# Performance work log

Measured on AMD Instinct MI355X. Metric: run time of the kernel, lower is better.

Reference implementation:

```python
import jax, jax.numpy as jnp
import numpy as np

B, N, D = 256, 196, 1024   # batch, regions, vis_embed_dim
HID, ATT, SIN, WID, ISD = 1024, 256, 1024, 1024, 256
S = 10                      # sentence steps


def _lin(key, out_dim, in_dim):
    kw, kb = jax.random.split(key)
    w = jax.random.normal(kw, (out_dim, in_dim), jnp.float32) * 0.02
    b = jax.random.normal(kb, (out_dim,), jnp.float32) * 0.02
    return w, b


def setup_inputs() -> dict:
    key = jax.random.key(0)
    ks = jax.random.split(key, 16)
    inp = {}
    inp['vis_enc'] = jax.random.normal(ks[0], (B, N, D), jnp.float32)
    inp['sentences'] = jax.random.randint(ks[1], (B, S, 50), 0, 10000, jnp.int64)
    inp['enc_att_w'], inp['enc_att_b'] = _lin(ks[2], ATT, D)
    inp['dec_att_w'], inp['dec_att_b'] = _lin(ks[3], ATT, HID)
    inp['full_att_w'], inp['full_att_b'] = _lin(ks[4], 1, ATT)
    inp['ctx_w'], inp['ctx_b'] = _lin(ks[5], SIN, D)
    inp['W_ih'], inp['b_ih'] = _lin(ks[6], 4 * HID, SIN)
    inp['W_hh'], inp['b_hh'] = _lin(ks[7], 4 * HID, HID)
    inp['topic_hid_w'], inp['topic_hid_b'] = _lin(ks[8], WID, HID)
    inp['topic_ctx_w'], inp['topic_ctx_b'] = _lin(ks[9], WID, SIN)
    inp['stop_prev_w'], inp['stop_prev_b'] = _lin(ks[10], ISD, HID)
    inp['stop_cur_w'], inp['stop_cur_b'] = _lin(ks[11], ISD, HID)
    inp['final_stop_w'], inp['final_stop_b'] = _lin(ks[12], 2, ISD)
    return inp


def reference(vis_enc, sentences,
              enc_att_w, enc_att_b, dec_att_w, dec_att_b, full_att_w, full_att_b,
              ctx_w, ctx_b, W_ih, b_ih, W_hh, b_hh,
              topic_hid_w, topic_hid_b, topic_ctx_w, topic_ctx_b,
              stop_prev_w, stop_prev_b, stop_cur_w, stop_cur_b,
              final_stop_w, final_stop_b):
    batch, hid = vis_enc.shape[0], W_hh.shape[1]
    sent_num = sentences.shape[1]
    # encoder projection is h-independent -> hoist out of the recurrence
    vis_enc_att = jnp.einsum('bnd,ad->bna', vis_enc, enc_att_w) + enc_att_b  # [B,N,ATT]

    def step(carry, _):
        h, c = carry
        # CoAtt additive attention
        dec = h @ dec_att_w.T + dec_att_b                       # [B,ATT]
        join = jnp.tanh(vis_enc_att + dec[:, None, :])          # [B,N,ATT]
        logits = jnp.einsum('bna,a->bn', join, full_att_w[0]) + full_att_b[0]
        scores = jax.nn.softmax(logits, axis=1)                 # [B,N]
        att_out = jnp.einsum('bn,bnd->bd', scores, vis_enc)     # [B,D]
        ctx = att_out @ ctx_w.T + ctx_b                         # [B,SIN]
        h_prev = h
        # LSTMCell
        gates = ctx @ W_ih.T + b_ih + h @ W_hh.T + b_hh         # [B,4H]
        i, f, g, o = jnp.split(gates, 4, axis=1)
        c_new = jax.nn.sigmoid(f) * c + jax.nn.sigmoid(i) * jnp.tanh(g)
        h_new = jax.nn.sigmoid(o) * jnp.tanh(c_new)
        # topic + stop heads
        topic = jnp.tanh(h_new @ topic_hid_w.T + topic_hid_b
                         + ctx @ topic_ctx_w.T + topic_ctx_b)   # [B,WID]
        p = jnp.tanh(h_prev @ stop_prev_w.T + stop_prev_b
                     + h_new @ stop_cur_w.T + stop_cur_b)
        p = p @ final_stop_w.T + final_stop_b                   # [B,2]
        return (h_new, c_new), (topic, p)

    h0 = jnp.zeros((batch, hid), vis_enc.dtype)
    c0 = jnp.zeros((batch, hid), vis_enc.dtype)
    _, (topics, ps) = jax.lax.scan(step, (h0, c0), None, length=sent_num)
    topics = jnp.transpose(topics, (1, 0, 2))  # [B,S,WID]
    ps = jnp.transpose(ps, (1, 0, 2))          # [B,S,2]
    return topics, ps
```

## Files before the change

### kernel.cpp

```cpp
#include <hip/hip_runtime.h>
#include <hip/hip_bf16.h>
#include <math.h>

static constexpr int BB = 256;
static constexpr int NR = 196;
static constexpr int DV = 1024;
static constexpr int HH = 1024;
static constexpr int AT = 256;
static constexpr int SI = 1024;
static constexpr int WI = 1024;
static constexpr int IS = 256;
static constexpr int ST = 10;

__device__ __forceinline__ float sigmoidf_(float x) { return 1.0f / (1.0f + expf(-x)); }

__device__ __forceinline__ ushort f2bf(float x) {
    uint u = __float_as_uint(x);
    return (ushort)((u + 0x7FFFu + ((u >> 16) & 1u)) >> 16);
}
__device__ __forceinline__ float bf2f(ushort b) { return __uint_as_float(((uint)b) << 16); }

using bf16x8 = __attribute__((ext_vector_type(8))) short;
using f32x4  = __attribute__((ext_vector_type(4))) float;
#define MFMA_B16(a, b, c) __builtin_amdgcn_mfma_f32_16x16x32_bf16((a), (b), (c), 0, 0, 0)

__device__ __forceinline__ void split8(const float4& u, const float4& v, uint4& hq, uint4& lq) {
    ushort h0 = f2bf(u.x), h1 = f2bf(u.y), h2 = f2bf(u.z), h3 = f2bf(u.w);
    ushort h4 = f2bf(v.x), h5 = f2bf(v.y), h6 = f2bf(v.z), h7 = f2bf(v.w);
    hq.x = h0 | ((uint)h1 << 16); hq.y = h2 | ((uint)h3 << 16);
    hq.z = h4 | ((uint)h5 << 16); hq.w = h6 | ((uint)h7 << 16);
    ushort l0 = f2bf(u.x - bf2f(h0)), l1 = f2bf(u.y - bf2f(h1));
    ushort l2 = f2bf(u.z - bf2f(h2)), l3 = f2bf(u.w - bf2f(h3));
    ushort l4 = f2bf(v.x - bf2f(h4)), l5 = f2bf(v.y - bf2f(h5));
    ushort l6 = f2bf(v.z - bf2f(h6)), l7 = f2bf(v.w - bf2f(h7));
    lq.x = l0 | ((uint)l1 << 16); lq.y = l2 | ((uint)l3 << 16);
    lq.z = l4 | ((uint)l5 << 16); lq.w = l6 | ((uint)l7 << 16);
}

struct CvtTab { const float* s[5]; ushort* h[5]; ushort* l[5]; };

__global__ __launch_bounds__(256) void convert_split(CvtTab tab) {
    const int cum[6] = {0, 256, 4352, 5376, 5632, 5888};
    const int bid = blockIdx.x;
    int seg = 0;
#pragma unroll
    for (int i = 1; i < 5; ++i) if (bid >= cum[i]) seg = i;
    const float* s = tab.s[seg];
    ushort* h = tab.h[seg];
    ushort* l = tab.l[seg];
    const int r = bid - cum[seg];
    int rd = r;
    if (seg == 1) rd = (r & 1023) * 4 + (r >> 10);
    const int src = r * 1024 + threadIdx.x * 4;
    const size_t dst = (size_t)rd * 1024 + threadIdx.x * 4;
    float4 v = *(const float4*)(s + src);
    ushort h0 = f2bf(v.x), h1 = f2bf(v.y), h2 = f2bf(v.z), h3 = f2bf(v.w);
    uint2 hq, lq;
    hq.x = h0 | ((uint)h1 << 16); hq.y = h2 | ((uint)h3 << 16);
    ushort l0 = f2bf(v.x - bf2f(h0)), l1 = f2bf(v.y - bf2f(h1));
    ushort l2 = f2bf(v.z - bf2f(h2)), l3 = f2bf(v.w - bf2f(h3));
    lq.x = l0 | ((uint)l1 << 16); lq.y = l2 | ((uint)l3 << 16);
    *(uint2*)(h + dst) = hq;
    *(uint2*)(l + dst) = lq;
}

__global__ __launch_bounds__(256) void convert_vis(
    const float* __restrict__ src, ushort* __restrict__ dst)
{
    const size_t i = ((size_t)blockIdx.x * 256 + threadIdx.x) * 8;
    const float4 v0 = *(const float4*)(src + i);
    const float4 v1 = *(const float4*)(src + i + 4);
    uint4 o;
    o.x = f2bf(v0.x) | ((uint)f2bf(v0.y) << 16);
    o.y = f2bf(v0.z) | ((uint)f2bf(v0.w) << 16);
    o.z = f2bf(v1.x) | ((uint)f2bf(v1.y) << 16);
    o.w = f2bf(v1.z) | ((uint)f2bf(v1.w) << 16);
    *(uint4*)(dst + i) = o;
}

__global__ __launch_bounds__(256) void transpose_split(
    const float* __restrict__ src, ushort* __restrict__ dh, ushort* __restrict__ dl)
{
    __shared__ float T[32][33];
    const int tx = threadIdx.x & 31, ty = threadIdx.x >> 5;
    const int k0 = blockIdx.x * 32, n0 = blockIdx.y * 32;
#pragma unroll
    for (int j = 0; j < 4; ++j)
        T[ty + 8 * j][tx] = src[(size_t)(k0 + ty + 8 * j) * 1024 + n0 + tx];
    __syncthreads();
#pragma unroll
    for (int j = 0; j < 4; ++j) {
        const float v = T[tx][ty + 8 * j];
        const ushort h = f2bf(v);
        const size_t o = (size_t)(n0 + ty + 8 * j) * 1024 + k0 + tx;
        dh[o] = h;
        dl[o] = f2bf(v - bf2f(h));
    }
}

__global__ __launch_bounds__(256) void foldbias(
    const float* __restrict__ W, const float* __restrict__ v,
    const float* __restrict__ b, float* __restrict__ out)
{
    const int n = blockIdx.x * 4 + (threadIdx.x >> 6);
    const int lane = threadIdx.x & 63;
    const float* wr = W + (size_t)n * 1024;
    float p = 0.f;
#pragma unroll
    for (int i = 0; i < 4; ++i) {
        const float4 wv = *(const float4*)&wr[i * 256 + lane * 4];
        const float4 vv = *(const float4*)&v[i * 256 + lane * 4];
        p = fmaf(wv.x, vv.x, p); p = fmaf(wv.y, vv.y, p);
        p = fmaf(wv.z, vv.z, p); p = fmaf(wv.w, vv.w, p);
    }
    for (int off = 32; off; off >>= 1) p += __shfl_down(p, off);
    if (lane == 0) out[n] = p + b[n];
}

template <int ILV>
__global__ __launch_bounds__(256) void mgemm_ws(
    const float* __restrict__ A, const ushort* __restrict__ Wh, const ushort* __restrict__ Wl,
    ushort* __restrict__ Ch, ushort* __restrict__ Cl, int N, int K)
{
    __shared__ __align__(16) ushort SM[4 * 64 * 40];
    ushort* Ah = SM; ushort* Al = SM + 2560; ushort* Bh = SM + 5120; ushort* Bl = SM + 7680;

    const int t = threadIdx.x;
    const int m0 = blockIdx.y * 64, n0 = blockIdx.x * 64;
    const int w = t >> 6, lane = t & 63;
    const int l15 = lane & 15, q = lane >> 4;
    const int sr = t >> 2, sq = (t & 3) * 8;
    const int nch = K >> 5;

    f32x4 acc[4] = {};
    float4 pa0, pa1; uint4 pbh, pbl;
    auto pref = [&](int c) {
        const int k0 = c << 5;
        const float* ap = &A[(size_t)(m0 + sr) * K + k0 + sq];
        pa0 = *(const float4*)ap;
        pa1 = *(const float4*)(ap + 4);
        pbh = *(const uint4*)&Wh[(size_t)(n0 + sr) * K + k0 + sq];
        pbl = *(const uint4*)&Wl[(size_t)(n0 + sr) * K + k0 + sq];
    };
    pref(0);

    for (int c = 0; c < nch; ++c) {
        __syncthreads();
        uint4 hq, lq; split8(pa0, pa1, hq, lq);
        *(uint4*)&Ah[sr * 40 + sq] = hq;
        *(uint4*)&Al[sr * 40 + sq] = lq;
        *(uint4*)&Bh[sr * 40 + sq] = pbh;
        *(uint4*)&Bl[sr * 40 + sq] = pbl;
        __syncthreads();
        if (c + 1 < nch) pref(c + 1);
        const bf16x8 bh = *(const bf16x8*)&Bh[(w * 16 + l15) * 40 + q * 8];
        const bf16x8 bl = *(const bf16x8*)&Bl[(w * 16 + l15) * 40 + q * 8];
#pragma unroll
        for (int mi = 0; mi < 4; ++mi) {
            const bf16x8 ah = *(const bf16x8*)&Ah[(mi * 16 + l15) * 40 + q * 8];
            const bf16x8 al = *(const bf16x8*)&Al[(mi * 16 + l15) * 40 + q * 8];
            acc[mi] = MFMA_B16(ah, bh, acc[mi]);
            acc[mi] = MFMA_B16(ah, bl, acc[mi]);
            acc[mi] = MFMA_B16(al, bh, acc[mi]);
        }
    }

    const int col = n0 + w * 16 + l15;
#pragma unroll
    for (int mi = 0; mi < 4; ++mi) {
#pragma unroll
        for (int j = 0; j < 4; ++j) {
            const int row = m0 + mi * 16 + q * 4 + j;
            const int ro = ILV ? ((row & 1023) * 4 + (row >> 10)) : row;
            const float v = acc[mi][j];
            const ushort h = f2bf(v);
            Ch[(size_t)ro * N + col] = h;
            Cl[(size_t)ro * N + col] = f2bf(v - bf2f(h));
        }
    }
}

template <int EPI, int DUAL, int OMAP>
__global__ __launch_bounds__(256) void mgemm(
    const float* __restrict__ A1, const ushort* __restrict__ W1h, const ushort* __restrict__ W1l,
    const float* __restrict__ b1,
    const float* __restrict__ A2, const ushort* __restrict__ W2h, const ushort* __restrict__ W2l,
    const float* __restrict__ b2,
    float* __restrict__ C, int M, int N, int K, int ldc)
{
    __shared__ __align__(16) ushort SM[4 * 64 * 40];
    ushort* Ah = SM; ushort* Al = SM + 2560; ushort* Bh = SM + 5120; ushort* Bl = SM + 7680;

    const int t = threadIdx.x;
    const int m0 = blockIdx.y * 64, n0 = blockIdx.x * 64;
    const int w = t >> 6, lane = t & 63;
    const int l15 = lane & 15, q = lane >> 4;
    const int sr = t >> 2, sq = (t & 3) * 8;
    const int KC = K >> 5, nch = (DUAL ? 2 : 1) * KC;

    f32x4 acc[4] = {};
    float4 pa0, pa1; uint4 pbh, pbl;

    auto pref = [&](int c) {
        const int pass = DUAL ? (c >= KC ? 1 : 0) : 0;
        const int k0 = (c - pass * KC) << 5;
        const float* A = pass ? A2 : A1;
        const ushort* Wh = pass ? W2h : W1h;
        const ushort* Wl = pass ? W2l : W1l;
        const float* ap = &A[(size_t)(m0 + sr) * K + k0 + sq];
        pa0 = *(const float4*)ap;
        pa1 = *(const float4*)(ap + 4);
        pbh = *(const uint4*)&Wh[(size_t)(n0 + sr) * K + k0 + sq];
        pbl = *(const uint4*)&Wl[(size_t)(n0 + sr) * K + k0 + sq];
    };
    pref(0);

    for (int c = 0; c < nch; ++c) {
        __syncthreads();
        uint4 hq, lq; split8(pa0, pa1, hq, lq);
        *(uint4*)&Ah[sr * 40 + sq] = hq;
        *(uint4*)&Al[sr * 40 + sq] = lq;
        *(uint4*)&Bh[sr * 40 + sq] = pbh;
        *(uint4*)&Bl[sr * 40 + sq] = pbl;
        __syncthreads();
        if (c + 1 < nch) pref(c + 1);
        const bf16x8 bh = *(const bf16x8*)&Bh[(w * 16 + l15) * 40 + q * 8];
        const bf16x8 bl = *(const bf16x8*)&Bl[(w * 16 + l15) * 40 + q * 8];
#pragma unroll
        for (int mi = 0; mi < 4; ++mi) {
            const bf16x8 ah = *(const bf16x8*)&Ah[(mi * 16 + l15) * 40 + q * 8];
            const bf16x8 al = *(const bf16x8*)&Al[(mi * 16 + l15) * 40 + q * 8];
            acc[mi] = MFMA_B16(ah, bh, acc[mi]);
            acc[mi] = MFMA_B16(ah, bl, acc[mi]);
            acc[mi] = MFMA_B16(al, bh, acc[mi]);
        }
    }

    const int col = n0 + w * 16 + l15;
    float bias = b1[col];
    if (DUAL) bias += b2[col];
#pragma unroll
    for (int mi = 0; mi < 4; ++mi) {
#pragma unroll
        for (int j = 0; j < 4; ++j) {
            const int row = m0 + mi * 16 + q * 4 + j;
            float v = acc[mi][j] + bias;
            if (EPI == 1) v = tanhf(v);
            if (OMAP)
                C[((size_t)(row & 255) * ST + (row >> 8)) * ldc + col] = v;
            else
                C[(size_t)row * ldc + col] = v;
        }
    }
}

__global__ __launch_bounds__(512) void mgemm8_lstm(
    const ushort* __restrict__ A1h, const ushort* __restrict__ A1l,
    const ushort* __restrict__ W1h, const ushort* __restrict__ W1l,
    const float* __restrict__ b1,
    const ushort* __restrict__ A2h, const ushort* __restrict__ A2l,
    const ushort* __restrict__ W2h, const ushort* __restrict__ W2l,
    const float* __restrict__ b2,
    int K, float* __restrict__ cvec, float* __restrict__ hnew,
    ushort* __restrict__ hnh, ushort* __restrict__ hnl)
{
    __shared__ __align__(16) ushort SM[32256];

    const int t = threadIdx.x;
    const int m0 = blockIdx.y * 64, n0 = blockIdx.x * 32;
    const int w = t >> 6, lane = t & 63;
    const int g = w >> 2, wg = w & 3;
    const int l15 = lane & 15, q = lane >> 4;
    const int tl = t & 255;
    const int sr = tl >> 2, sq4 = (tl & 3) * 16;
    const int br = tl >> 3, bq = (tl & 7) * 8;
    const int mh = wg >> 1;
    const int colL = (wg & 1) * 16 + l15;

    ushort* Ah = SM + g * 13824;
    ushort* Al = Ah + 4608;
    ushort* Bh = Al + 4608;
    ushort* Bl = Bh + 2304;

    const int nchg = K >> 6;
    const ushort* Ahg = g ? A2h : A1h;
    const ushort* Alg = g ? A2l : A1l;
    const ushort* Wh  = g ? W2h : W1h;
    const ushort* Wl  = g ? W2l : W1l;

    f32x4 acc[2] = {};
    uint4 pah0, pah1, pal0, pal1, pbh, pbl;
    auto pref = [&](int c) {
        const int k0 = c << 6;
        const size_t ab = (size_t)(m0 + sr) * K + k0 + sq4;
        pah0 = *(const uint4*)&Ahg[ab];
        pah1 = *(const uint4*)&Ahg[ab + 8];
        pal0 = *(const uint4*)&Alg[ab];
        pal1 = *(const uint4*)&Alg[ab + 8];
        pbh = *(const uint4*)&Wh[(size_t)(n0 + br) * K + k0 + bq];
        pbl = *(const uint4*)&Wl[(size_t)(n0 + br) * K + k0 + bq];
    };
    pref(0);

    for (int c = 0; c < nchg; ++c) {
        __syncthreads();
        *(uint4*)&Ah[sr * 72 + sq4]     = pah0;
        *(uint4*)&Ah[sr * 72 + sq4 + 8] = pah1;
        *(uint4*)&Al[sr * 72 + sq4]     = pal0;
        *(uint4*)&Al[sr * 72 + sq4 + 8] = pal1;
        *(uint4*)&Bh[br * 72 + bq] = pbh;
        *(uint4*)&Bl[br * 72 + bq] = pbl;
        __syncthreads();
        if (c + 1 < nchg) pref(c + 1);
#pragma unroll
        for (int ks = 0; ks < 2; ++ks) {
            const bf16x8 bh = *(const bf16x8*)&Bh[colL * 72 + ks * 32 + q * 8];
            const bf16x8 bl = *(const bf16x8*)&Bl[colL * 72 + ks * 32 + q * 8];
#pragma unroll
            for (int i = 0; i < 2; ++i) {
                const int mi = mh * 2 + i;
                const bf16x8 ah = *(const bf16x8*)&Ah[(mi * 16 + l15) * 72 + ks * 32 + q * 8];
                const bf16x8 al = *(const bf16x8*)&Al[(mi * 16 + l15) * 72 + ks * 32 + q * 8];
                acc[i] = MFMA_B16(ah, bh, acc[i]);
                acc[i] = MFMA_B16(ah, bl, acc[i]);
                acc[i] = MFMA_B16(al, bh, acc[i]);
            }
        }
    }

    float* comb = (float*)(SM + 27648);
    __syncthreads();
    if (g == 1) {
#pragma unroll
        for (int i = 0; i < 2; ++i)
#pragma unroll
            for (int j = 0; j < 4; ++j) comb[tl * 9 + i * 4 + j] = acc[i][j];
    }
    __syncthreads();
    if (g == 0) {
#pragma unroll
        for (int i = 0; i < 2; ++i)
#pragma unroll
            for (int j = 0; j < 4; ++j) acc[i][j] += comb[tl * 9 + i * 4 + j];
    }

    float* G = (float*)(SM + 13824);
    if (g == 0) {
        const int colG = n0 + colL;
        const int gate = colG & 3, unit = colG >> 2;
        const float bias = b1[gate * 1024 + unit] + b2[gate * 1024 + unit];
#pragma unroll
        for (int i = 0; i < 2; ++i) {
            const int mi = mh * 2 + i;
#pragma unroll
            for (int j = 0; j < 4; ++j)
                G[(mi * 16 + q * 4 + j) * 40 + colL] = acc[i][j] + bias;
        }
    }
    __syncthreads();
    {
        const int row = t >> 3, ul = t & 7;
        const float4 g4 = *(const float4*)&G[row * 40 + ul * 4];
        const size_t ci = (size_t)(m0 + row) * HH + (n0 >> 2) + ul;
        const float cn = sigmoidf_(g4.y) * cvec[ci] + sigmoidf_(g4.x) * tanhf(g4.z);
        cvec[ci] = cn;
        const float hv = sigmoidf_(g4.w) * tanhf(cn);
        hnew[ci] = hv;
        const ushort hhi = f2bf(hv);
        hnh[ci] = hhi;
        hnl[ci] = f2bf(hv - bf2f(hhi));
    }
}

__global__ __launch_bounds__(512) void mgemm_preb(
    const ushort* __restrict__ vh, const ushort* __restrict__ Wh, const ushort* __restrict__ Wl,
    const float* __restrict__ bias, ushort* __restrict__ C)
{
    __shared__ __align__(16) ushort Avh[128 * 40];
    __shared__ __align__(16) ushort Bh[256 * 40];
    __shared__ __align__(16) ushort Bl[256 * 40];

    const int t = threadIdx.x;
    const int m0 = blockIdx.x * 128;
    const int w = t >> 6, lane = t & 63;
    const int rg = w >> 2, cg = w & 3;
    const int l15 = lane & 15, q = lane >> 4;
    const int ar = t >> 2, ac = (t & 3) * 8;
    const int brr = t >> 1, bc = (t & 1) * 16;
    const int K = DV;

    f32x4 acc[4][4] = {};
    uint4 pa, pbh0, pbh1, pbl0, pbl1;
    auto pref = [&](int c) {
        const int k0 = c << 5;
        pa   = *(const uint4*)&vh[(size_t)(m0 + ar) * K + k0 + ac];
        const size_t bb = (size_t)brr * K + k0 + bc;
        pbh0 = *(const uint4*)&Wh[bb];
        pbh1 = *(const uint4*)&Wh[bb + 8];
        pbl0 = *(const uint4*)&Wl[bb];
        pbl1 = *(const uint4*)&Wl[bb + 8];
    };
    pref(0);

    for (int c = 0; c < 32; ++c) {
        __syncthreads();
        *(uint4*)&Avh[ar * 40 + ac] = pa;
        *(uint4*)&Bh[brr * 40 + bc]     = pbh0;
        *(uint4*)&Bh[brr * 40 + bc + 8] = pbh1;
        *(uint4*)&Bl[brr * 40 + bc]     = pbl0;
        *(uint4*)&Bl[brr * 40 + bc + 8] = pbl1;
        __syncthreads();
        if (c + 1 < 32) pref(c + 1);

        bf16x8 ah[4];
#pragma unroll
        for (int mi = 0; mi < 4; ++mi)
            ah[mi] = *(const bf16x8*)&Avh[(rg * 64 + mi * 16 + l15) * 40 + q * 8];
#pragma unroll
        for (int ni = 0; ni < 4; ++ni) {
            const bf16x8 bh = *(const bf16x8*)&Bh[(cg * 64 + ni * 16 + l15) * 40 + q * 8];
            const bf16x8 bl = *(const bf16x8*)&Bl[(cg * 64 + ni * 16 + l15) * 40 + q * 8];
#pragma unroll
            for (int mi = 0; mi < 4; ++mi) {
                acc[mi][ni] = MFMA_B16(ah[mi], bh, acc[mi][ni]);
                acc[mi][ni] = MFMA_B16(ah[mi], bl, acc[mi][ni]);
            }
        }
    }

#pragma unroll
    for (int ni = 0; ni < 4; ++ni) {
        const int col = cg * 64 + ni * 16 + l15;
        const float bb = bias[col];
#pragma unroll
        for (int mi = 0; mi < 4; ++mi)
#pragma unroll
            for (int j = 0; j < 4; ++j) {
                const int row = m0 + rg * 64 + mi * 16 + q * 4 + j;
                C[(size_t)row * AT + col] = f2bf(acc[mi][ni][j] + bb);
            }
    }
}

__global__ __launch_bounds__(256) void mgemm_pre(
    const float* __restrict__ A, const ushort* __restrict__ Wh, const ushort* __restrict__ Wl,
    const float* __restrict__ bias, ushort* __restrict__ C)
{
    __shared__ __align__(16) ushort Ah[64 * 40], Al[64 * 40];
    __shared__ __align__(16) ushort Bh[256 * 40], Bl[256 * 40];

    const int t = threadIdx.x;
    const int m0 = blockIdx.x * 64;
    const int w = t >> 6, lane = t & 63;
    const int l15 = lane & 15, q = lane >> 4;
    const int sr = t >> 2, sq = (t & 3) * 8;
    const int K = DV;

    f32x4 acc[4][4] = {};
    float4 pa0, pa1;
    auto prefA = [&](int k0) {
        const float* ap = &A[(size_t)(m0 + sr) * K + k0 + sq];
        pa0 = *(const float4*)ap;
        pa1 = *(const float4*)(ap + 4);
    };
    prefA(0);

    for (int c = 0; c < 32; ++c) {
        const int k0 = c << 5;
        __syncthreads();
        uint4 hq, lq; split8(pa0, pa1, hq, lq);
        *(uint4*)&Ah[sr * 40 + sq] = hq;
        *(uint4*)&Al[sr * 40 + sq] = lq;
#pragma unroll
        for (int i = 0; i < 4; ++i) {
            const int r = sr + 64 * i;
            *(uint4*)&Bh[r * 40 + sq] = *(const uint4*)&Wh[(size_t)r * K + k0 + sq];
            *(uint4*)&Bl[r * 40 + sq] = *(const uint4*)&Wl[(size_t)r * K + k0 + sq];
        }
        __syncthreads();
        if (c + 1 < 32) prefA((c + 1) << 5);

        bf16x8 ah[4], al[4];
#pragma unroll
        for (int mi = 0; mi < 4; ++mi) {
            ah[mi] = *(const bf16x8*)&Ah[(mi * 16 + l15) * 40 + q * 8];
            al[mi] = *(const bf16x8*)&Al[(mi * 16 + l15) * 40 + q * 8];
        }
#pragma unroll
        for (int ni = 0; ni < 4; ++ni) {
            const bf16x8 bh = *(const bf16x8*)&Bh[(w * 64 + ni * 16 + l15) * 40 + q * 8];
            const bf16x8 bl = *(const bf16x8*)&Bl[(w * 64 + ni * 16 + l15) * 40 + q * 8];
#pragma unroll
            for (int mi = 0; mi < 4; ++mi) {
                acc[mi][ni] = MFMA_B16(ah[mi], bh, acc[mi][ni]);
                acc[mi][ni] = MFMA_B16(ah[mi], bl, acc[mi][ni]);
                acc[mi][ni] = MFMA_B16(al[mi], bh, acc[mi][ni]);
            }
        }
    }

#pragma unroll
    for (int ni = 0; ni < 4; ++ni) {
        const int col = w * 64 + ni * 16 + l15;
        const float bb = bias[col];
#pragma unroll
        for (int mi = 0; mi < 4; ++mi)
#pragma unroll
            for (int j = 0; j < 4; ++j) {
                const int row = m0 + mi * 16 + q * 4 + j;
                C[(size_t)row * AT + col] = f2bf(acc[mi][ni][j] + bb);
            }
    }
}

template <int VBF>
__global__ __launch_bounds__(1024) void att_step(
    const ushort* __restrict__ vis_att, const float* __restrict__ h,
    const float* __restrict__ dec_w, const float* __restrict__ dec_b,
    const float* __restrict__ fw, const float* __restrict__ fbp,
    const void* __restrict__ visp, float* __restrict__ att_out,
    ushort* __restrict__ att_h, ushort* __restrict__ att_l)
{
    const int b = blockIdx.x;
    const int t = threadIdx.x;
    const int lane = t & 63;
    const int w = t >> 6;

    __shared__ float hs[HH];
    __shared__ float decs[AT];
    __shared__ float fwv[AT];
    __shared__ float logit[NR + 4];
    __shared__ float sc[NR + 4];
    __shared__ float red[8];
    __shared__ float part[8][DV];

    hs[t] = h[(size_t)b * HH + t];
    if (t < AT) fwv[t] = fw[t];
    __syncthreads();
    const float fb = fbp[0];

#pragma unroll
    for (int j = 0; j < 16; ++j) {
        const int a = w * 16 + j;
        const float* wr = dec_w + (size_t)a * HH;
        float p = 0.f;
#pragma unroll
        for (int i = 0; i < 4; ++i) {
            const float4 wv = *(const float4*)&wr[i * 256 + lane * 4];
            const float4 hv = *(const float4*)&hs[i * 256 + lane * 4];
            p = fmaf(wv.x, hv.x, p); p = fmaf(wv.y, hv.y, p);
            p = fmaf(wv.z, hv.z, p); p = fmaf(wv.w, hv.w, p);
        }
        for (int off = 32; off; off >>= 1) p += __shfl_down(p, off);
        if (lane == 0) decs[a] = p + dec_b[a];
    }
    __syncthreads();

    for (int n = w; n < NR; n += 16) {
        const ushort4 v4 = *(const ushort4*)&vis_att[((size_t)b * NR + n) * AT + lane * 4];
        const int a = lane * 4;
        float s = tanhf(bf2f(v4.x) + decs[a]) * fwv[a];
        s = fmaf(tanhf(bf2f(v4.y) + decs[a + 1]), fwv[a + 1], s);
        s = fmaf(tanhf(bf2f(v4.z) + decs[a + 2]), fwv[a + 2], s);
        s = fmaf(tanhf(bf2f(v4.w) + decs[a + 3]), fwv[a + 3], s);
        for (int off = 32; off; off >>= 1) s += __shfl_down(s, off);
        if (lane == 0) logit[n] = s + fb;
    }
    __syncthreads();

    float m = -1e30f, e = 0.f;
    if (t < NR) m = logit[t];
    if (t < 256) {
        for (int off = 32; off; off >>= 1) m = fmaxf(m, __shfl_down(m, off));
        if (lane == 0) red[w] = m;
    }
    __syncthreads();
    m = fmaxf(fmaxf(red[0], red[1]), fmaxf(red[2], red[3]));
    if (t < NR) e = expf(logit[t] - m);
    if (t < 256) {
        float ss = e;
        for (int off = 32; off; off >>= 1) ss += __shfl_down(ss, off);
        if (lane == 0) red[4 + w] = ss;
    }
    __syncthreads();
    const float S = red[4] + red[5] + red[6] + red[7];
    if (t < NR) sc[t] = e / S;
    __syncthreads();

    const int slice = t >> 7;
    const int c8 = (t & 127) * 8;
    const int nbeg = (slice <= 4) ? 25 * slice : 100 + 24 * (slice - 4);
    const int nend = (slice < 4) ? nbeg + 25 : nbeg + 24;
    float a0 = 0.f, a1 = 0.f, a2 = 0.f, a3 = 0.f;
    float a4 = 0.f, a5 = 0.f, a6 = 0.f, a7 = 0.f;
    if (VBF) {
        const ushort* vb = (const ushort*)visp + (size_t)b * NR * DV + c8;
        for (int n = nbeg; n < nend; ++n) {
            const float s = sc[n];
            const uint4 v = *(const uint4*)&vb[(size_t)n * DV];
            a0 = fmaf(s, bf2f((ushort)(v.x & 0xFFFF)), a0);
            a1 = fmaf(s, bf2f((ushort)(v.x >> 16)), a1);
            a2 = fmaf(s, bf2f((ushort)(v.y & 0xFFFF)), a2);
            a3 = fmaf(s, bf2f((ushort)(v.y >> 16)), a3);
            a4 = fmaf(s, bf2f((ushort)(v.z & 0xFFFF)), a4);
            a5 = fmaf(s, bf2f((ushort)(v.z >> 16)), a5);
            a6 = fmaf(s, bf2f((ushort)(v.w & 0xFFFF)), a6);
            a7 = fmaf(s, bf2f((ushort)(v.w >> 16)), a7);
        }
    } else {
        const float* vb = (const float*)visp + (size_t)b * NR * DV + c8;
        for (int n = nbeg; n < nend; ++n) {
            const float s = sc[n];
            const float4 v0 = *(const float4*)&vb[(size_t)n * DV];
            const float4 v1 = *(const float4*)&vb[(size_t)n * DV + 4];
            a0 = fmaf(s, v0.x, a0); a1 = fmaf(s, v0.y, a1);
            a2 = fmaf(s, v0.z, a2); a3 = fmaf(s, v0.w, a3);
            a4 = fmaf(s, v1.x, a4); a5 = fmaf(s, v1.y, a5);
            a6 = fmaf(s, v1.z, a6); a7 = fmaf(s, v1.w, a7);
        }
    }
    float4 av0; av0.x = a0; av0.y = a1; av0.z = a2; av0.w = a3;
    float4 av1; av1.x = a4; av1.y = a5; av1.z = a6; av1.w = a7;
    *(float4*)&part[slice][c8]     = av0;
    *(float4*)&part[slice][c8 + 4] = av1;
    __syncthreads();
    const float v = ((part[0][t] + part[1][t]) + (part[2][t] + part[3][t]))
                  + ((part[4][t] + part[5][t]) + (part[6][t] + part[7][t]));
    att_out[(size_t)b * DV + t] = v;
    const ushort vh16 = f2bf(v);
    att_h[(size_t)b * DV + t] = vh16;
    att_l[(size_t)b * DV + t] = f2bf(v - bf2f(vh16));
}

__global__ __launch_bounds__(256) void stop_final_all(
    const float* __restrict__ pt, const float* __restrict__ fw,
    const float* __restrict__ fb, float* __restrict__ outp)
{
    const int row = blockIdx.x;
    const int s = row >> 8, b = row & 255;
    const int t = threadIdx.x;
    const int lane = t & 63;
    const int w = t >> 6;

    __shared__ float red[16];
    const float v = pt[(size_t)row * IS + t];
    float p0 = v * fw[t];
    float p1 = v * fw[IS + t];
    for (int off = 32; off; off >>= 1) {
        p0 += __shfl_down(p0, off);
        p1 += __shfl_down(p1, off);
    }
    if (lane == 0) { red[w] = p0; red[8 + w] = p1; }
    __syncthreads();
    if (t == 0) {
        outp[((size_t)b * ST + s) * 2 + 0] = red[0] + red[1] + red[2] + red[3] + fb[0];
        outp[((size_t)b * ST + s) * 2 + 1] = red[8] + red[9] + red[10] + red[11] + fb[1];
    }
}

extern "C" void kernel_launch(void* const* d_in, const int* in_sizes, int n_in,
                              void* d_out, int out_size, void* d_ws, size_t ws_size,
                              hipStream_t stream)
{
    const float* vis        = (const float*)d_in[0];
    const float* enc_att_w  = (const float*)d_in[2];
    const float* enc_att_b  = (const float*)d_in[3];
    const float* dec_att_w  = (const float*)d_in[4];
    const float* dec_att_b  = (const float*)d_in[5];
    const float* full_att_w = (const float*)d_in[6];
    const float* full_att_b = (const float*)d_in[7];
    const float* ctx_w      = (const float*)d_in[8];
    const float* ctx_b      = (const float*)d_in[9];
    const float* W_ih       = (const float*)d_in[10];
    const float* b_ih       = (const float*)d_in[11];
    const float* W_hh       = (const float*)d_in[12];
    const float* b_hh       = (const float*)d_in[13];
    const float* topic_hid_w = (const float*)d_in[14];
    const float* topic_hid_b = (const float*)d_in[15];
    const float* topic_ctx_w = (const float*)d_in[16];
    const float* topic_ctx_b = (const float*)d_in[17];
    const float* stop_prev_w = (const float*)d_in[18];
    const float* stop_prev_b = (const float*)d_in[19];
    const float* stop_cur_w  = (const float*)d_in[20];
    const float* stop_cur_b  = (const float*)d_in[21];
    const float* final_stop_w = (const float*)d_in[22];
    const float* final_stop_b = (const float*)d_in[23];

    float* out_topics = (float*)d_out;
    float* out_ps     = (float*)d_out + (size_t)BB * ST * WI;

    char* ws = (char*)d_ws;
    size_t off = 0;
    auto alloc = [&](size_t bytes) -> void* {
        void* p = (void*)(ws + off);
        off += (bytes + 255) & ~(size_t)255;
        return p;
    };
    ushort* vis_att = (ushort*)alloc((size_t)BB * NR * AT * 2);
    const size_t WTOT = (size_t)5888 * 1024;
    ushort* wh = (ushort*)alloc(WTOT * 2);
    ushort* wl = (ushort*)alloc(WTOT * 2);
    float* h_all   = (float*)alloc((size_t)(ST + 1) * BB * HH * 4);
    ushort* hh_h   = (ushort*)alloc((size_t)(ST + 1) * BB * HH * 2);
    ushort* hh_l   = (ushort*)alloc((size_t)(ST + 1) * BB * HH * 2);
    float* att_all = (float*)alloc((size_t)ST * BB * DV * 4);
    ushort* att_h  = (ushort*)alloc((size_t)BB * DV * 2);
    ushort* att_l  = (ushort*)alloc((size_t)BB * DV * 2);
    float* cbuf    = (float*)alloc((size_t)BB * HH * 4);
    float* pt_all  = (float*)alloc((size_t)ST * BB * IS * 4);
    ushort* ctT_h  = (ushort*)alloc((size_t)SI * DV * 2);
    ushort* ctT_l  = (ushort*)alloc((size_t)SI * DV * 2);
    ushort* cmb_h  = (ushort*)alloc((size_t)4 * HH * SI * 2);
    ushort* cmb_l  = (ushort*)alloc((size_t)4 * HH * SI * 2);
    ushort* tcc_h  = (ushort*)alloc((size_t)WI * SI * 2);
    ushort* tcc_l  = (ushort*)alloc((size_t)WI * SI * 2);
    float* bf_ih   = (float*)alloc((size_t)4 * HH * 4);
    float* bf_tc   = (float*)alloc((size_t)WI * 4);
    if (off > ws_size) return;
    ushort* vis_bf = nullptr;
    {
        const size_t need = (size_t)BB * NR * DV * 2;
        if (off + need <= ws_size) vis_bf = (ushort*)alloc(need);
    }

    const size_t O_ENC = 0;
    const size_t O_HH  = 262144;
    const size_t O_TH  = 4456448;
    const size_t O_SP  = 5505024;
    const size_t O_SC  = 5767168;

    CvtTab tab;
    const float* srcs[5] = {enc_att_w, W_hh, topic_hid_w, stop_prev_w, stop_cur_w};
    const size_t offs[5] = {O_ENC, O_HH, O_TH, O_SP, O_SC};
    for (int i = 0; i < 5; ++i) {
        tab.s[i] = srcs[i];
        tab.h[i] = wh + offs[i];
        tab.l[i] = wl + offs[i];
    }

    hipMemsetAsync(h_all, 0, (size_t)BB * HH * 4, stream);
    hipMemsetAsync(hh_h, 0, (size_t)BB * HH * 2, stream);
    hipMemsetAsync(hh_l, 0, (size_t)BB * HH * 2, stream);
    hipMemsetAsync(cbuf, 0, (size_t)BB * HH * 4, stream);

    convert_split<<<5888, 256, 0, stream>>>(tab);

    transpose_split<<<dim3(SI / 32, DV / 32), 256, 0, stream>>>(ctx_w, ctT_h, ctT_l);
    mgemm_ws<1><<<dim3(SI / 64, 4 * HH / 64), 256, 0, stream>>>(
        W_ih, ctT_h, ctT_l, cmb_h, cmb_l, SI, DV);
    mgemm_ws<0><<<dim3(SI / 64, WI / 64), 256, 0, stream>>>(
        topic_ctx_w, ctT_h, ctT_l, tcc_h, tcc_l, SI, DV);
    foldbias<<<(4 * HH) / 4, 256, 0, stream>>>(W_ih, ctx_b, b_ih, bf_ih);
    foldbias<<<WI / 4, 256, 0, stream>>>(topic_ctx_w, ctx_b, topic_ctx_b, bf_tc);

    if (vis_bf) {
        convert_vis<<<(BB * NR * DV) / (256 * 8), 256, 0, stream>>>(vis, vis_bf);
        mgemm_preb<<<(BB * NR) / 128, 512, 0, stream>>>(
            vis_bf, wh + O_ENC, wl + O_ENC, enc_att_b, vis_att);
    } else {
        mgemm_pre<<<(BB * NR) / 64, 256, 0, stream>>>(
            vis, wh + O_ENC, wl + O_ENC, enc_att_b, vis_att);
    }

    for (int s = 0; s < ST; ++s) {
        float* hc = h_all + (size_t)s * BB * HH;
        float* hn = h_all + (size_t)(s + 1) * BB * HH;
        ushort* hch = hh_h + (size_t)s * BB * HH;
        ushort* hcl = hh_l + (size_t)s * BB * HH;
        ushort* hnh = hh_h + (size_t)(s + 1) * BB * HH;
        ushort* hnl = hh_l + (size_t)(s + 1) * BB * HH;
        float* atts = att_all + (size_t)s * BB * DV;
        if (vis_bf)
            att_step<1><<<BB, 1024, 0, stream>>>(vis_att, hc, dec_att_w, dec_att_b,
                                                 full_att_w, full_att_b, vis_bf, atts,
                                                 att_h, att_l);
        else
            att_step<0><<<BB, 1024, 0, stream>>>(vis_att, hc, dec_att_w, dec_att_b,
                                                 full_att_w, full_att_b, vis, atts,
                                                 att_h, att_l);
        mgemm8_lstm<<<dim3(4 * HH / 32, BB / 64), 512, 0, stream>>>(
            att_h, att_l, cmb_h, cmb_l, bf_ih,
            hch, hcl, wh + O_HH, wl + O_HH, b_hh,
            SI, cbuf, hn, hnh, hnl);
    }

    mgemm<1, 1, 1><<<dim3(WI / 64, (ST * BB) / 64), 256, 0, stream>>>(
        h_all + (size_t)BB * HH, wh + O_TH, wl + O_TH, topic_hid_b,
        att_all, tcc_h, tcc_l, bf_tc,
        out_topics, ST * BB, WI, HH, WI);
    mgemm<1, 1, 0><<<dim3(IS / 64, (ST * BB) / 64), 256, 0, stream>>>(
        h_all, wh + O_SP, wl + O_SP, stop_prev_b,
        h_all + (size_t)BB * HH, wh + O_SC, wl + O_SC, stop_cur_b,
        pt_all, ST * BB, IS, HH, IS);
    stop_final_all<<<ST * BB, 256, 0, stream>>>(pt_all, final_stop_w, final_stop_b, out_ps);
}
```

Measured before the change: 1.073 ms.

## Reuse pre-split bf16 activations in head GEMMs and swizzle LSTM weight LDS

The topic and stop head GEMMs now read the pre-split bf16 hi/lo copies of h and the attention output instead of fp32 inputs, so the per-chunk split conversion disappears. Attention output is stored only as bf16 hi/lo per step, which drops the fp32 att_all write. The LSTM GEMM B tile gets an XOR-swizzled LDS layout with no padding, a smaller shared footprint and a launch_bounds occupancy hint. The fp32 fallback path is removed, so the bf16 vis workspace must now always be available.

New measurement: 1.035 ms. -3.6%, faster.

```diff
diff --git a/kernel.cpp b/kernel.cpp
--- a/kernel.cpp
+++ b/kernel.cpp
@@ -180,13 +180,15 @@
     }
 }
 
-template <int EPI, int DUAL, int OMAP>
-__global__ __launch_bounds__(256) void mgemm(
-    const float* __restrict__ A1, const ushort* __restrict__ W1h, const ushort* __restrict__ W1l,
+template <int OMAP>
+__global__ __launch_bounds__(256) void mgemm_ps(
+    const ushort* __restrict__ A1h, const ushort* __restrict__ A1l,
+    const ushort* __restrict__ W1h, const ushort* __restrict__ W1l,
     const float* __restrict__ b1,
-    const float* __restrict__ A2, const ushort* __restrict__ W2h, const ushort* __restrict__ W2l,
+    const ushort* __restrict__ A2h, const ushort* __restrict__ A2l,
+    const ushort* __restrict__ W2h, const ushort* __restrict__ W2l,
     const float* __restrict__ b2,
-    float* __restrict__ C, int M, int N, int K, int ldc)
+    float* __restrict__ C, int N, int K, int ldc)
 {
     __shared__ __align__(16) ushort SM[4 * 64 * 40];
     ushort* Ah = SM; ushort* Al = SM + 2560; ushort* Bh = SM + 5120; ushort* Bl = SM + 7680;
@@ -196,20 +198,21 @@
     const int w = t >> 6, lane = t & 63;
     const int l15 = lane & 15, q = lane >> 4;
     const int sr = t >> 2, sq = (t & 3) * 8;
-    const int KC = K >> 5, nch = (DUAL ? 2 : 1) * KC;
+    const int KC = K >> 5, nch = 2 * KC;
 
     f32x4 acc[4] = {};
-    float4 pa0, pa1; uint4 pbh, pbl;
+    uint4 pah, pal, pbh, pbl;
 
     auto pref = [&](int c) {
-        const int pass = DUAL ? (c >= KC ? 1 : 0) : 0;
+        const int pass = (c >= KC) ? 1 : 0;
         const int k0 = (c - pass * KC) << 5;
-        const float* A = pass ? A2 : A1;
+        const ushort* Axh = pass ? A2h : A1h;
+        const ushort* Axl = pass ? A2l : A1l;
         const ushort* Wh = pass ? W2h : W1h;
         const ushort* Wl = pass ? W2l : W1l;
-        const float* ap = &A[(size_t)(m0 + sr) * K + k0 + sq];
-        pa0 = *(const float4*)ap;
-        pa1 = *(const float4*)(ap + 4);
+        const size_t ab = (size_t)(m0 + sr) * K + k0 + sq;
+        pah = *(const uint4*)&Axh[ab];
+        pal = *(const uint4*)&Axl[ab];
         pbh = *(const uint4*)&Wh[(size_t)(n0 + sr) * K + k0 + sq];
         pbl = *(const uint4*)&Wl[(size_t)(n0 + sr) * K + k0 + sq];
     };
@@ -217,9 +220,8 @@
 
     for (int c = 0; c < nch; ++c) {
         __syncthreads();
-        uint4 hq, lq; split8(pa0, pa1, hq, lq);
-        *(uint4*)&Ah[sr * 40 + sq] = hq;
-        *(uint4*)&Al[sr * 40 + sq] = lq;
+        *(uint4*)&Ah[sr * 40 + sq] = pah;
+        *(uint4*)&Al[sr * 40 + sq] = pal;
         *(uint4*)&Bh[sr * 40 + sq] = pbh;
         *(uint4*)&Bl[sr * 40 + sq] = pbl;
         __syncthreads();
@@ -237,15 +239,13 @@
     }
 
     const int col = n0 + w * 16 + l15;
-    float bias = b1[col];
-    if (DUAL) bias += b2[col];
+    const float bias = b1[col] + b2[col];
 #pragma unroll
     for (int mi = 0; mi < 4; ++mi) {
 #pragma unroll
         for (int j = 0; j < 4; ++j) {
             const int row = m0 + mi * 16 + q * 4 + j;
-            float v = acc[mi][j] + bias;
-            if (EPI == 1) v = tanhf(v);
+            const float v = tanhf(acc[mi][j] + bias);
             if (OMAP)
                 C[((size_t)(row & 255) * ST + (row >> 8)) * ldc + col] = v;
             else
@@ -254,7 +254,7 @@
     }
 }
 
-__global__ __launch_bounds__(512) void mgemm8_lstm(
+__global__ __launch_bounds__(512, 6) void mgemm8_lstm(
     const ushort* __restrict__ A1h, const ushort* __restrict__ A1l,
     const ushort* __restrict__ W1h, const ushort* __restrict__ W1l,
     const float* __restrict__ b1,
@@ -264,7 +264,7 @@
     int K, float* __restrict__ cvec, float* __restrict__ hnew,
     ushort* __restrict__ hnh, ushort* __restrict__ hnl)
 {
-    __shared__ __align__(16) ushort SM[32256];
+    __shared__ __align__(16) ushort SM[26624];
 
     const int t = threadIdx.x;
     const int m0 = blockIdx.y * 64, n0 = blockIdx.x * 32;
@@ -277,16 +277,18 @@
     const int mh = wg >> 1;
     const int colL = (wg & 1) * 16 + l15;
 
-    ushort* Ah = SM + g * 13824;
+    ushort* Ah = SM + g * 13312;
     ushort* Al = Ah + 4608;
     ushort* Bh = Al + 4608;
-    ushort* Bl = Bh + 2304;
+    ushort* Bl = Bh + 2048;
 
     const int nchg = K >> 6;
     const ushort* Ahg = g ? A2h : A1h;
     const ushort* Alg = g ? A2l : A1l;
     const ushort* Wh  = g ? W2h : W1h;
     const ushort* Wl  = g ? W2l : W1l;
+
+    const int bwi = br * 64 + (bq ^ ((br & 7) << 3));
 
     f32x4 acc[2] = {};
     uint4 pah0, pah1, pal0, pal1, pbh, pbl;
@@ -308,14 +310,15 @@
         *(uint4*)&Ah[sr * 72 + sq4 + 8] = pah1;
         *(uint4*)&Al[sr * 72 + sq4]     = pal0;
         *(uint4*)&Al[sr * 72 + sq4 + 8] = pal1;
-        *(uint4*)&Bh[br * 72 + bq] = pbh;
-        *(uint4*)&Bl[br * 72 + bq] = pbl;
+        *(uint4*)&Bh[bwi] = pbh;
+        *(uint4*)&Bl[bwi] = pbl;
         __syncthreads();
         if (c + 1 < nchg) pref(c + 1);
 #pragma unroll
         for (int ks = 0; ks < 2; ++ks) {
-            const bf16x8 bh = *(const bf16x8*)&Bh[colL * 72 + ks * 32 + q * 8];
-            const bf16x8 bl = *(const bf16x8*)&Bl[colL * 72 + ks * 32 + q * 8];
+            const int bro = colL * 64 + ((ks * 32 + q * 8) ^ ((colL & 7) << 3));
+            const bf16x8 bh = *(const bf16x8*)&Bh[bro];
+            const bf16x8 bl = *(const bf16x8*)&Bl[bro];
 #pragma unroll
             for (int i = 0; i < 2; ++i) {
                 const int mi = mh * 2 + i;
@@ -328,7 +331,7 @@
         }
     }
 
-    float* comb = (float*)(SM + 27648);
+    float* comb = (float*)(SM + 13312);
     __syncthreads();
     if (g == 1) {
 #pragma unroll
@@ -344,7 +347,7 @@
             for (int j = 0; j < 4; ++j) acc[i][j] += comb[tl * 9 + i * 4 + j];
     }
 
-    float* G = (float*)(SM + 13824);
+    float* G = (float*)(SM + 17920);
     if (g == 0) {
         const int colG = n0 + colL;
         const int gate = colG & 3, unit = colG >> 2;
@@ -442,83 +445,12 @@
     }
 }
 
-__global__ __launch_bounds__(256) void mgemm_pre(
-    const float* __restrict__ A, const ushort* __restrict__ Wh, const ushort* __restrict__ Wl,
-    const float* __restrict__ bias, ushort* __restrict__ C)
-{
-    __shared__ __align__(16) ushort Ah[64 * 40], Al[64 * 40];
-    __shared__ __align__(16) ushort Bh[256 * 40], Bl[256 * 40];
-
-    const int t = threadIdx.x;
-    const int m0 = blockIdx.x * 64;
-    const int w = t >> 6, lane = t & 63;
-    const int l15 = lane & 15, q = lane >> 4;
-    const int sr = t >> 2, sq = (t & 3) * 8;
-    const int K = DV;
-
-    f32x4 acc[4][4] = {};
-    float4 pa0, pa1;
-    auto prefA = [&](int k0) {
-        const float* ap = &A[(size_t)(m0 + sr) * K + k0 + sq];
-        pa0 = *(const float4*)ap;
-        pa1 = *(const float4*)(ap + 4);
-    };
-    prefA(0);
-
-    for (int c = 0; c < 32; ++c) {
-        const int k0 = c << 5;
-        __syncthreads();
-        uint4 hq, lq; split8(pa0, pa1, hq, lq);
-        *(uint4*)&Ah[sr * 40 + sq] = hq;
-        *(uint4*)&Al[sr * 40 + sq] = lq;
-#pragma unroll
-        for (int i = 0; i < 4; ++i) {
-            const int r = sr + 64 * i;
-            *(uint4*)&Bh[r * 40 + sq] = *(const uint4*)&Wh[(size_t)r * K + k0 + sq];
-            *(uint4*)&Bl[r * 40 + sq] = *(const uint4*)&Wl[(size_t)r * K + k0 + sq];
-        }
-        __syncthreads();
-        if (c + 1 < 32) prefA((c + 1) << 5);
-
-        bf16x8 ah[4], al[4];
-#pragma unroll
-        for (int mi = 0; mi < 4; ++mi) {
-            ah[mi] = *(const bf16x8*)&Ah[(mi * 16 + l15) * 40 + q * 8];
-            al[mi] = *(const bf16x8*)&Al[(mi * 16 + l15) * 40 + q * 8];
-        }
-#pragma unroll
-        for (int ni = 0; ni < 4; ++ni) {
-            const bf16x8 bh = *(const bf16x8*)&Bh[(w * 64 + ni * 16 + l15) * 40 + q * 8];
-            const bf16x8 bl = *(const bf16x8*)&Bl[(w * 64 + ni * 16 + l15) * 40 + q * 8];
-#pragma unroll
-            for (int mi = 0; mi < 4; ++mi) {
-                acc[mi][ni] = MFMA_B16(ah[mi], bh, acc[mi][ni]);
-                acc[mi][ni] = MFMA_B16(ah[mi], bl, acc[mi][ni]);
-                acc[mi][ni] = MFMA_B16(al[mi], bh, acc[mi][ni]);
-            }
-        }
-    }
-
-#pragma unroll
-    for (int ni = 0; ni < 4; ++ni) {
-        const int col = w * 64 + ni * 16 + l15;
-        const float bb = bias[col];
-#pragma unroll
-        for (int mi = 0; mi < 4; ++mi)
-#pragma unroll
-            for (int j = 0; j < 4; ++j) {
-                const int row = m0 + mi * 16 + q * 4 + j;
-                C[(size_t)row * AT + col] = f2bf(acc[mi][ni][j] + bb);
-            }
-    }
-}
-
 template <int VBF>
 __global__ __launch_bounds__(1024) void att_step(
     const ushort* __restrict__ vis_att, const float* __restrict__ h,
     const float* __restrict__ dec_w, const float* __restrict__ dec_b,
     const float* __restrict__ fw, const float* __restrict__ fbp,
-    const void* __restrict__ visp, float* __restrict__ att_out,
+    const void* __restrict__ visp,
     ushort* __restrict__ att_h, ushort* __restrict__ att_l)
 {
     const int b = blockIdx.x;
@@ -626,7 +558,6 @@
     __syncthreads();
     const float v = ((part[0][t] + part[1][t]) + (part[2][t] + part[3][t]))
                   + ((part[4][t] + part[5][t]) + (part[6][t] + part[7][t]));
-    att_out[(size_t)b * DV + t] = v;
     const ushort vh16 = f2bf(v);
     att_h[(size_t)b * DV + t] = vh16;
     att_l[(size_t)b * DV + t] = f2bf(v - bf2f(vh16));
@@ -703,9 +634,8 @@
     float* h_all   = (float*)alloc((size_t)(ST + 1) * BB * HH * 4);
     ushort* hh_h   = (ushort*)alloc((size_t)(ST + 1) * BB * HH * 2);
     ushort* hh_l   = (ushort*)alloc((size_t)(ST + 1) * BB * HH * 2);
-    float* att_all = (float*)alloc((size_t)ST * BB * DV * 4);
-    ushort* att_h  = (ushort*)alloc((size_t)BB * DV * 2);
-    ushort* att_l  = (ushort*)alloc((size_t)BB * DV * 2);
+    ushort* att_all_h = (ushort*)alloc((size_t)ST * BB * DV * 2);
+    ushort* att_all_l = (ushort*)alloc((size_t)ST * BB * DV * 2);
     float* cbuf    = (float*)alloc((size_t)BB * HH * 4);
     float* pt_all  = (float*)alloc((size_t)ST * BB * IS * 4);
     ushort* ctT_h  = (ushort*)alloc((size_t)SI * DV * 2);
@@ -753,14 +683,9 @@
     foldbias<<<(4 * HH) / 4, 256, 0, stream>>>(W_ih, ctx_b, b_ih, bf_ih);
     foldbias<<<WI / 4, 256, 0, stream>>>(topic_ctx_w, ctx_b, topic_ctx_b, bf_tc);
 
-    if (vis_bf) {
-        convert_vis<<<(BB * NR * DV) / (256 * 8), 256, 0, stream>>>(vis, vis_bf);
-        mgemm_preb<<<(BB * NR) / 128, 512, 0, stream>>>(
-            vis_bf, wh + O_ENC, wl + O_ENC, enc_att_b, vis_att);
-    } else {
-        mgemm_pre<<<(BB * NR) / 64, 256, 0, stream>>>(
-            vis, wh + O_ENC, wl + O_ENC, enc_att_b, vis_att);
-    }
+    convert_vis<<<(BB * NR * DV) / (256 * 8), 256, 0, stream>>>(vis, vis_bf);
+    mgemm_preb<<<(BB * NR) / 128, 512, 0, stream>>>(
+        vis_bf, wh + O_ENC, wl + O_ENC, enc_att_b, vis_att);
 
     for (int s = 0; s < ST; ++s) {
         float* hc = h_all + (size_t)s * BB * HH;
@@ -769,28 +694,26 @@
         ushort* hcl = hh_l + (size_t)s * BB * HH;
         ushort* hnh = hh_h + (size_t)(s + 1) * BB * HH;
         ushort* hnl = hh_l + (size_t)(s + 1) * BB * HH;
-        float* atts = att_all + (size_t)s * BB * DV;
-        if (vis_bf)
-            att_step<1><<<BB, 1024, 0, stream>>>(vis_att, hc, dec_att_w, dec_att_b,
-                                                 full_att_w, full_att_b, vis_bf, atts,
-                                                 att_h, att_l);
-        else
-            att_step<0><<<BB, 1024, 0, stream>>>(vis_att, hc, dec_att_w, dec_att_b,
-                                                 full_att_w, full_att_b, vis, atts,
-                                                 att_h, att_l);
+        ushort* ath = att_all_h + (size_t)s * BB * DV;
+        ushort* atl = att_all_l + (size_t)s * BB * DV;
+        att_step<1><<<BB, 1024, 0, stream>>>(vis_att, hc, dec_att_w, dec_att_b,
+                                             full_att_w, full_att_b, vis_bf,
+                                             ath, atl);
         mgemm8_lstm<<<dim3(4 * HH / 32, BB / 64), 512, 0, stream>>>(
-            att_h, att_l, cmb_h, cmb_l, bf_ih,
+            ath, atl, cmb_h, cmb_l, bf_ih,
             hch, hcl, wh + O_HH, wl + O_HH, b_hh,
             SI, cbuf, hn, hnh, hnl);
     }
 
-    mgemm<1, 1, 1><<<dim3(WI / 64, (ST * BB) / 64), 256, 0, stream>>>(
-        h_all + (size_t)BB * HH, wh + O_TH, wl + O_TH, topic_hid_b,
-        att_all, tcc_h, tcc_l, bf_tc,
-        out_topics, ST * BB, WI, HH, WI);
-    mgemm<1, 1, 0><<<dim3(IS / 64, (ST * BB) / 64), 256, 0, stream>>>(
-        h_all, wh + O_SP, wl + O_SP, stop_prev_b,
-        h_all + (size_t)BB * HH, wh + O_SC, wl + O_SC, stop_cur_b,
-        pt_all, ST * BB, IS, HH, IS);
+    mgemm_ps<1><<<dim3(WI / 64, (ST * BB) / 64), 256, 0, stream>>>(
+        hh_h + (size_t)BB * HH, hh_l + (size_t)BB * HH,
+        wh + O_TH, wl + O_TH, topic_hid_b,
+        att_all_h, att_all_l, tcc_h, tcc_l, bf_tc,
+        out_topics, WI, HH, WI);
+    mgemm_ps<0><<<dim3(IS / 64, (ST * BB) / 64), 256, 0, stream>>>(
+        hh_h, hh_l, wh + O_SP, wl + O_SP, stop_prev_b,
+        hh_h + (size_t)BB * HH, hh_l + (size_t)BB * HH,
+        wh + O_SC, wl + O_SC, stop_cur_b,
+        pt_all, IS, HH, IS);
     stop_final_all<<<ST * BB, 256, 0, stream>>>(pt_all, final_stop_w, final_stop_b, out_ps);
 }
```
